# Performance work log

Hardware: AMD Instinct MI355X
Metric: run time of the kernel (lower is better)

## Reference

```python
import jax, jax.numpy as jnp
import numpy as np

N_NODES = 50000
N_EDGES = 1600000
IN_FEAT = 128
OUT_FEAT = 128


def setup_inputs() -> dict:
    key = jax.random.key(0)
    k_x, k_w, k_v, k_r, k_c = jax.random.split(key, 5)
    X = jax.random.normal(k_x, (N_NODES, IN_FEAT), dtype=jnp.float32)
    # nn.Linear(in_feat, out_feat, bias=False) weight: [out_feat, in_feat]
    W = jax.random.normal(k_w, (OUT_FEAT, IN_FEAT), dtype=jnp.float32) * (1.0 / np.sqrt(IN_FEAT))
    # Sparse adjacency A in COO form: A[rows[e], cols[e]] = vals[e]
    A_vals = jax.random.uniform(k_v, (N_EDGES,), dtype=jnp.float32)
    A_rows = jax.random.randint(k_r, (N_EDGES,), 0, N_NODES, dtype=jnp.int32)
    A_cols = jax.random.randint(k_c, (N_EDGES,), 0, N_NODES, dtype=jnp.int32)
    return {"X": X, "W": W, "A_vals": A_vals, "A_rows": A_rows, "A_cols": A_cols}


def reference(X, W, A_vals, A_rows, A_cols):
    # H = linear(X) = X @ W.T  -> [N, out_feat]
    H = jnp.einsum("ni,oi->no", X, W)
    # out = A @ H via COO SpMM: gather source rows, scale by edge value,
    # scatter-add into destination rows.
    msgs = A_vals[:, None] * H[A_cols]            # [E, out_feat]
    out = jax.ops.segment_sum(msgs, A_rows, num_segments=N_NODES)
    return out
```

## Files before the change

kernel.cpp:

```cpp
#include <hip/hip_runtime.h>


constexpr int N_NODES = 50000;
constexpr int N_EDGES = 1600000;
constexpr int FEAT    = 128;

constexpr int ROWS_PER_BIN = 64;
constexpr int NB           = (N_NODES + ROWS_PER_BIN - 1) / ROWS_PER_BIN;
constexpr int CAP          = 2560;
constexpr int CHUNK        = 4096;
constexpr int EPT          = 4;
constexpr int PART_BLOCKS  = (N_EDGES + CHUNK - 1) / CHUNK;
constexpr int GEMM_BLOCKS  = (N_NODES + 255) / 256;
constexpr int FUSED_GROUPS = 196;
constexpr int FUSED_BLOCKS = FUSED_GROUPS * 3;
constexpr int OVF_CAP      = 8192;

constexpr int PITCH = 136;

typedef short short8 __attribute__((ext_vector_type(8)));
typedef float f32x4  __attribute__((ext_vector_type(4)));

__device__ __forceinline__ unsigned short f2bf(float x) {
    unsigned u = __float_as_uint(x);
    u += 0x7fffu + ((u >> 16) & 1u);
    return (unsigned short)(u >> 16);
}
__device__ __forceinline__ float bf2f(unsigned short s) {
    return __uint_as_float(((unsigned)s) << 16);
}

__device__ __forceinline__ float dec_val10(unsigned w) {
    return (float)(w & 1023u) * (1.0f / 1023.0f);
}

__device__ void gemm_body(const float* __restrict__ X, const float* __restrict__ W,
                          unsigned short* __restrict__ Hb, int g,
                          unsigned short* Wsh) {
    const int tid  = threadIdx.x;
    const int row0 = g * 256;

#pragma unroll
    for (int t = 0; t < 4; t++) {
        int idx = tid + 1024 * t;
        int r   = idx >> 5;
        int c4  = (idx & 31) << 2;
        const float4 v = *(const float4*)&W[r * FEAT + c4];
        unsigned lo = f2bf(v.x) | ((unsigned)f2bf(v.y) << 16);
        unsigned hi = f2bf(v.z) | ((unsigned)f2bf(v.w) << 16);
        *(uint2*)&Wsh[r * PITCH + c4] = make_uint2(lo, hi);
    }
    __syncthreads();

    const int w    = tid >> 6;
    const int lane = tid & 63;
    const int n    = lane & 15;
    const int q    = lane >> 4;

    f32x4 acc[8];
#pragma unroll
    for (int t = 0; t < 8; t++) acc[t] = (f32x4){0.f, 0.f, 0.f, 0.f};

    int xrow = row0 + 16 * w + n;
    if (xrow >= N_NODES) xrow = N_NODES - 1;
    const float* xp = X + (size_t)xrow * FEAT;

#pragma unroll
    for (int kt = 0; kt < 4; kt++) {
        const int ko = kt * 32 + q * 8;
        const float4 a0 = *(const float4*)&xp[ko];
        const float4 a1 = *(const float4*)&xp[ko + 4];
        short8 bfrag;
        bfrag[0] = (short)f2bf(a0.x); bfrag[1] = (short)f2bf(a0.y);
        bfrag[2] = (short)f2bf(a0.z); bfrag[3] = (short)f2bf(a0.w);
        bfrag[4] = (short)f2bf(a1.x); bfrag[5] = (short)f2bf(a1.y);
        bfrag[6] = (short)f2bf(a1.z); bfrag[7] = (short)f2bf(a1.w);
#pragma unroll
        for (int t = 0; t < 8; t++) {
            const short8 afrag = *(const short8*)&Wsh[(16 * t + n) * PITCH + ko];
            acc[t] = __builtin_amdgcn_mfma_f32_16x16x32_bf16(afrag, bfrag, acc[t], 0, 0, 0);
        }
    }

    const int grow = row0 + 16 * w + n;
    if (grow < N_NODES) {
#pragma unroll
        for (int t = 0; t < 8; t++) {
            ushort4 pk;
            pk.x = f2bf(acc[t][0]); pk.y = f2bf(acc[t][1]);
            pk.z = f2bf(acc[t][2]); pk.w = f2bf(acc[t][3]);
            *(ushort4*)&Hb[grow * FEAT + 16 * t + 4 * q] = pk;
        }
    }
}

__device__ void partition_body(const int* __restrict__ rows, const int* __restrict__ cols,
                               const float* __restrict__ vals,
                               int* __restrict__ gcur, unsigned* __restrict__ binbuf,
                               int* __restrict__ ovf_cnt, int* __restrict__ ovf,
                               int g, int* smem) {
    int* hist  = smem;
    int* wbase = smem + NB;
    const int tid = threadIdx.x;
    const int e0  = g * CHUNK;

    for (int i = tid; i < NB; i += 1024) hist[i] = 0;
    __syncthreads();

    int      myrow[EPT], myrank[EPT];
    unsigned myword[EPT];
#pragma unroll
    for (int t = 0; t < EPT; t++) {
        int e = e0 + t * 1024 + tid;
        if (e < N_EDGES) {
            int r = rows[e];
            unsigned vq = (unsigned)__float2int_rn(vals[e] * 1023.0f);
            myrow[t]  = r;
            myword[t] = ((unsigned)(r & 63) << 26) | ((unsigned)cols[e] << 10) | vq;
            myrank[t] = atomicAdd(&hist[r >> 6], 1);
        } else {
            myrow[t] = -1; myword[t] = 0; myrank[t] = 0;
        }
    }
    __syncthreads();

    for (int i = tid; i < NB; i += 1024) {
        int c = hist[i];
        wbase[i] = (c > 0) ? atomicAdd(&gcur[i], c) : 0;
    }
    __syncthreads();

#pragma unroll
    for (int t = 0; t < EPT; t++) {
        int r = myrow[t];
        if (r < 0) continue;
        int b    = r >> 6;
        int rank = wbase[b] + myrank[t];
        if (rank < CAP) {
            binbuf[(size_t)b * CAP + rank] = myword[t];
        } else {
            int k = atomicAdd(ovf_cnt, 1);
            if (k < OVF_CAP) ovf[k] = e0 + t * 1024 + tid;
        }
    }
}

__global__ __launch_bounds__(1024) void gemm_partition(
    const float* __restrict__ X, const float* __restrict__ W,
    unsigned short* __restrict__ Hb,
    const int* __restrict__ rows, const int* __restrict__ cols,
    const float* __restrict__ vals,
    int* __restrict__ gcur, unsigned* __restrict__ binbuf,
    int* __restrict__ ovf_cnt, int* __restrict__ ovf) {
    __shared__ unsigned short Wsh[128 * PITCH];
    const int grp = blockIdx.x / 3;
    const int rem = blockIdx.x - grp * 3;
    if (rem == 2) {
        gemm_body(X, W, Hb, grp, Wsh);
    } else {
        int pg = grp * 2 + rem;
        if (pg < PART_BLOCKS)
            partition_body(rows, cols, vals, gcur, binbuf, ovf_cnt, ovf, pg, (int*)Wsh);
    }
}

__global__ __launch_bounds__(512) void spmm_bins(
    const int* __restrict__ gcur, const unsigned* __restrict__ binbuf,
    const unsigned short* __restrict__ Hb, float* __restrict__ out) {
    __shared__ unsigned sorted[CAP];
    __shared__ int hist[ROWS_PER_BIN];
    __shared__ int cnt_of[ROWS_PER_BIN];
    __shared__ int cur[ROWS_PER_BIN];

    const int b    = blockIdx.x;
    const int tid  = threadIdx.x;
    const int lane = tid & 63;
    const int w    = tid >> 6;

    if (tid < ROWS_PER_BIN) { hist[tid] = 0; cur[tid] = 0; }
    __syncthreads();

    int cnt = gcur[b];
    if (cnt > CAP) cnt = CAP;
    const unsigned* bb = binbuf + (size_t)b * CAP;

    for (int i = tid; i < cnt; i += 512)
        atomicAdd(&hist[bb[i] >> 26], 1);
    __syncthreads();

    if (w == 0) {
        int c = hist[lane];
        cnt_of[lane] = c;
        int v = c;
#pragma unroll
        for (int off = 1; off < 64; off <<= 1) {
            int u = __shfl_up(v, off);
            if (lane >= off) v += u;
        }
        hist[lane] = v - c;
    }
    __syncthreads();

    for (int i = tid; i < cnt; i += 512) {
        unsigned m = bb[i];
        int rl  = (int)(m >> 26);
        int pos = hist[rl] + atomicAdd(&cur[rl], 1);
        unsigned col = (m >> 10) & 0xffffu;
        unsigned vb  = (unsigned)f2bf(dec_val10(m));
        sorted[pos] = (vb << 16) | col;
    }
    __syncthreads();

    const int row0 = b * ROWS_PER_BIN;
    const ushort2* __restrict__ Hb2 = (const ushort2*)Hb;
    float2* out2 = (float2*)out;

    for (int rr = 0; rr < 8; rr++) {
        const int rl = w * 8 + rr;
        const int gr = row0 + rl;
        if (gr >= N_NODES) break;
        const int s = hist[rl];
        const int e = s + cnt_of[rl];

        float accx = 0.f, accy = 0.f;
        int i = s;
        for (; i + 16 <= e; i += 16) {
            float v[16];
            ushort2 h[16];
#pragma unroll
            for (int j = 0; j < 16; j++) {
                unsigned m = sorted[i + j];
                int col = (int)(m & 0xffffu);
                v[j] = __uint_as_float(m & 0xffff0000u);
                h[j] = Hb2[col * 64 + lane];
            }
#pragma unroll
            for (int j = 0; j < 16; j++) {
                accx += v[j] * bf2f(h[j].x);
                accy += v[j] * bf2f(h[j].y);
            }
        }
        for (; i + 4 <= e; i += 4) {
            float v[4];
            ushort2 h[4];
#pragma unroll
            for (int j = 0; j < 4; j++) {
                unsigned m = sorted[i + j];
                int col = (int)(m & 0xffffu);
                v[j] = __uint_as_float(m & 0xffff0000u);
                h[j] = Hb2[col * 64 + lane];
            }
#pragma unroll
            for (int j = 0; j < 4; j++) {
                accx += v[j] * bf2f(h[j].x);
                accy += v[j] * bf2f(h[j].y);
            }
        }
        for (; i < e; i++) {
            unsigned m = sorted[i];
            int col = (int)(m & 0xffffu);
            float vv = __uint_as_float(m & 0xffff0000u);
            ushort2 hh = Hb2[col * 64 + lane];
            accx += vv * bf2f(hh.x);
            accy += vv * bf2f(hh.y);
        }
        out2[gr * 64 + lane] = make_float2(accx, accy);
    }
}

__global__ void fixup_ovf(const int* __restrict__ ovf_cnt, const int* __restrict__ ovf,
                          const int* __restrict__ rows, const int* __restrict__ cols,
                          const float* __restrict__ vals,
                          const unsigned short* __restrict__ Hb, float* __restrict__ out) {
    int n = *ovf_cnt;
    if (n > OVF_CAP) n = OVF_CAP;
    for (int k = blockIdx.x; k < n; k += gridDim.x) {
        int e = ovf[k];
        int r = rows[e], c = cols[e];
        float v = vals[e];
        for (int f = threadIdx.x; f < FEAT; f += blockDim.x)
            atomicAdd(&out[r * FEAT + f], v * bf2f(Hb[c * FEAT + f]));
    }
}

__global__ __launch_bounds__(1024) void gemm_only(
    const float* __restrict__ X, const float* __restrict__ W,
    unsigned short* __restrict__ Hb) {
    __shared__ unsigned short Wsh[128 * PITCH];
    gemm_body(X, W, Hb, blockIdx.x, Wsh);
}

__global__ __launch_bounds__(256) void spmm_push_atomic(
    const int* __restrict__ rows, const int* __restrict__ cols,
    const float* __restrict__ vals, const unsigned short* __restrict__ Hb,
    float* __restrict__ out) {
    const int e    = blockIdx.x * 4 + (threadIdx.x >> 6);
    const int lane = threadIdx.x & 63;
    if (e >= N_EDGES) return;
    int r = rows[e], c = cols[e];
    float v = vals[e];
    atomicAdd(&out[r * FEAT + lane],      v * bf2f(Hb[c * FEAT + lane]));
    atomicAdd(&out[r * FEAT + 64 + lane], v * bf2f(Hb[c * FEAT + 64 + lane]));
}

extern "C" void kernel_launch(void* const* d_in, const int* in_sizes, int n_in,
                              void* d_out, int out_size, void* d_ws, size_t ws_size,
                              hipStream_t stream) {
    const float* X      = (const float*)d_in[0];
    const float* W      = (const float*)d_in[1];
    const float* A_vals = (const float*)d_in[2];
    const int*   A_rows = (const int*)d_in[3];
    const int*   A_cols = (const int*)d_in[4];
    float* out = (float*)d_out;

    auto align256 = [](size_t x) { return (x + 255) & ~size_t(255); };
    char* ws = (char*)d_ws;

    size_t off = 0;
    size_t hb_off   = off; off += align256(size_t(N_NODES) * FEAT * 2);
    size_t gcur_off = off; off += align256(size_t(NB) * sizeof(int));
    size_t ovfc_off = off; off += 256;
    size_t ovf_off  = off; off += align256(size_t(OVF_CAP) * sizeof(int));
    size_t bin_off  = off; off += size_t(NB) * CAP * sizeof(unsigned);
    const size_t need = off;

    unsigned short* Hb = (unsigned short*)(ws + hb_off);

    if (ws_size >= need) {
        int*      gcur    = (int*)(ws + gcur_off);
        int*      ovf_cnt = (int*)(ws + ovfc_off);
        int*      ovf     = (int*)(ws + ovf_off);
        unsigned* binbuf  = (unsigned*)(ws + bin_off);

        hipMemsetAsync(ws + gcur_off, 0, (ovfc_off - gcur_off) + 256, stream);
        gemm_partition<<<FUSED_BLOCKS, 1024, 0, stream>>>(X, W, Hb, A_rows, A_cols, A_vals,
                                                          gcur, binbuf, ovf_cnt, ovf);
        spmm_bins<<<NB, 512, 0, stream>>>(gcur, binbuf, Hb, out);
        fixup_ovf<<<16, 256, 0, stream>>>(ovf_cnt, ovf, A_rows, A_cols, A_vals, Hb, out);
    } else {
        gemm_only<<<GEMM_BLOCKS, 1024, 0, stream>>>(X, W, Hb);
        hipMemsetAsync(out, 0, size_t(N_NODES) * FEAT * sizeof(float), stream);
        spmm_push_atomic<<<(N_EDGES + 3) / 4, 256, 0, stream>>>(A_rows, A_cols, A_vals, Hb, out);
    }
}
```

Baseline: 171.5 us.

## Split SpMM bins across feature quarters and enlarge partition chunks

The SpMM kernel now launches four blocks per row bin. Each block handles a 32-feature quarter, and each wavefront works on four edges at once in 16-lane slots, combining the slots with cross-lane shuffles and writing output with nontemporal stores. This exposes more parallelism and more independent gathers per wavefront, but every block repeats the per-bin histogram and local sort, so that work and the binbuf reads are done four times. Separately, the partition phase processes 8192-edge chunks with 8 edges per thread, and the fused launch now alternates one partition block with one GEMM block.

```diff
diff --git a/kernel.cpp b/kernel.cpp
--- a/kernel.cpp
+++ b/kernel.cpp
@@ -8,18 +8,18 @@
 constexpr int ROWS_PER_BIN = 64;
 constexpr int NB           = (N_NODES + ROWS_PER_BIN - 1) / ROWS_PER_BIN;
 constexpr int CAP          = 2560;
-constexpr int CHUNK        = 4096;
-constexpr int EPT          = 4;
+constexpr int CHUNK        = 8192;
+constexpr int EPT          = 8;
 constexpr int PART_BLOCKS  = (N_EDGES + CHUNK - 1) / CHUNK;
 constexpr int GEMM_BLOCKS  = (N_NODES + 255) / 256;
-constexpr int FUSED_GROUPS = 196;
-constexpr int FUSED_BLOCKS = FUSED_GROUPS * 3;
+constexpr int FUSED_BLOCKS = PART_BLOCKS + GEMM_BLOCKS;
 constexpr int OVF_CAP      = 8192;
 
 constexpr int PITCH = 136;
 
 typedef short short8 __attribute__((ext_vector_type(8)));
 typedef float f32x4  __attribute__((ext_vector_type(4)));
+typedef float f32x2  __attribute__((ext_vector_type(2)));
 
 __device__ __forceinline__ unsigned short f2bf(float x) {
     unsigned u = __float_as_uint(x);
@@ -153,14 +153,12 @@
     int* __restrict__ gcur, unsigned* __restrict__ binbuf,
     int* __restrict__ ovf_cnt, int* __restrict__ ovf) {
     __shared__ unsigned short Wsh[128 * PITCH];
-    const int grp = blockIdx.x / 3;
-    const int rem = blockIdx.x - grp * 3;
-    if (rem == 2) {
+    const int grp = blockIdx.x >> 1;
+    if (blockIdx.x & 1) {
         gemm_body(X, W, Hb, grp, Wsh);
     } else {
-        int pg = grp * 2 + rem;
-        if (pg < PART_BLOCKS)
-            partition_body(rows, cols, vals, gcur, binbuf, ovf_cnt, ovf, pg, (int*)Wsh);
+        if (grp < PART_BLOCKS)
+            partition_body(rows, cols, vals, gcur, binbuf, ovf_cnt, ovf, grp, (int*)Wsh);
     }
 }
 
@@ -172,7 +170,9 @@
     __shared__ int cnt_of[ROWS_PER_BIN];
     __shared__ int cur[ROWS_PER_BIN];
 
-    const int b    = blockIdx.x;
+    const int bid  = blockIdx.x;
+    const int q    = (bid & 7) >> 1;
+    const int b    = (bid >> 3) * 2 + (bid & 1);
     const int tid  = threadIdx.x;
     const int lane = tid & 63;
     const int w    = tid >> 6;
@@ -211,8 +211,10 @@
     }
     __syncthreads();
 
-    const int row0 = b * ROWS_PER_BIN;
-    const ushort2* __restrict__ Hb2 = (const ushort2*)Hb;
+    const int row0   = b * ROWS_PER_BIN;
+    const int slot   = lane >> 4;
+    const int lane16 = lane & 15;
+    const ushort2* __restrict__ Hq = (const ushort2*)Hb + q * 16 + lane16;
     float2* out2 = (float2*)out;
 
     for (int rr = 0; rr < 8; rr++) {
@@ -225,46 +227,34 @@
         float accx = 0.f, accy = 0.f;
         int i = s;
         for (; i + 16 <= e; i += 16) {
-            float v[16];
-            ushort2 h[16];
-#pragma unroll
-            for (int j = 0; j < 16; j++) {
-                unsigned m = sorted[i + j];
-                int col = (int)(m & 0xffffu);
-                v[j] = __uint_as_float(m & 0xffff0000u);
-                h[j] = Hb2[col * 64 + lane];
+            float   vv[4];
+            ushort2 hh[4];
+#pragma unroll
+            for (int u = 0; u < 4; u++) {
+                unsigned m = sorted[i + u * 4 + slot];
+                vv[u] = __uint_as_float(m & 0xffff0000u);
+                hh[u] = Hq[(int)(m & 0xffffu) * 64];
             }
 #pragma unroll
-            for (int j = 0; j < 16; j++) {
-                accx += v[j] * bf2f(h[j].x);
-                accy += v[j] * bf2f(h[j].y);
+            for (int u = 0; u < 4; u++) {
+                accx += vv[u] * bf2f(hh[u].x);
+                accy += vv[u] * bf2f(hh[u].y);
             }
         }
-        for (; i + 4 <= e; i += 4) {
-            float v[4];
-            ushort2 h[4];
-#pragma unroll
-            for (int j = 0; j < 4; j++) {
-                unsigned m = sorted[i + j];
-                int col = (int)(m & 0xffffu);
-                v[j] = __uint_as_float(m & 0xffff0000u);
-                h[j] = Hb2[col * 64 + lane];
-            }
-#pragma unroll
-            for (int j = 0; j < 4; j++) {
-                accx += v[j] * bf2f(h[j].x);
-                accy += v[j] * bf2f(h[j].y);
-            }
-        }
-        for (; i < e; i++) {
-            unsigned m = sorted[i];
-            int col = (int)(m & 0xffffu);
-            float vv = __uint_as_float(m & 0xffff0000u);
-            ushort2 hh = Hb2[col * 64 + lane];
-            accx += vv * bf2f(hh.x);
-            accy += vv * bf2f(hh.y);
-        }
-        out2[gr * 64 + lane] = make_float2(accx, accy);
+        for (; i < e; i += 4) {
+            int idx = i + slot;
+            unsigned m = (idx < e) ? sorted[idx] : 0u;
+            float v2 = __uint_as_float(m & 0xffff0000u);
+            ushort2 h2 = Hq[(int)(m & 0xffffu) * 64];
+            accx += v2 * bf2f(h2.x);
+            accy += v2 * bf2f(h2.y);
+        }
+        accx += __shfl_xor(accx, 16); accy += __shfl_xor(accy, 16);
+        accx += __shfl_xor(accx, 32); accy += __shfl_xor(accy, 32);
+        if (slot == 0) {
+            f32x2 r; r[0] = accx; r[1] = accy;
+            __builtin_nontemporal_store(r, (f32x2*)&out2[(size_t)gr * 64 + q * 16 + lane16]);
+        }
     }
 }
 
@@ -335,7 +325,7 @@
         hipMemsetAsync(ws + gcur_off, 0, (ovfc_off - gcur_off) + 256, stream);
         gemm_partition<<<FUSED_BLOCKS, 1024, 0, stream>>>(X, W, Hb, A_rows, A_cols, A_vals,
                                                           gcur, binbuf, ovf_cnt, ovf);
-        spmm_bins<<<NB, 512, 0, stream>>>(gcur, binbuf, Hb, out);
+        spmm_bins<<<NB * 4, 512, 0, stream>>>(gcur, binbuf, Hb, out);
         fixup_ovf<<<16, 256, 0, stream>>>(ovf_cnt, ovf, A_rows, A_cols, A_vals, Hb, out);
     } else {
         gemm_only<<<GEMM_BLOCKS, 1024, 0, stream>>>(X, W, Hb);
```

Result: slower. 187.3 us (+9.2%).
